# Performance work log

Hardware: AMD Instinct MI355X
Metric: run time of the kernel (lower is better)

Reference implementation:

```python
import jax, jax.numpy as jnp
import numpy as np
from jax import lax

B, M, L, D, V, H, DEC_HID = 1024, 4, 100, 512, 50000, 512, 128


def setup_inputs() -> dict:
    key = jax.random.key(0)
    ks = jax.random.split(key, 16)
    inputs = jax.random.randint(ks[0], (B, M, L), 0, V)
    masks = (jax.random.uniform(ks[1], (B, M)) > 0.3).astype(jnp.float32)
    embed_table = jax.random.normal(ks[2], (V, D), dtype=jnp.float32) * 0.02
    s_d = 1.0 / np.sqrt(D)
    s_h = 1.0 / np.sqrt(H)
    # torch nn.RNN params: h_t = relu(x W_ih^T + b_ih + h_{t-1} W_hh^T + b_hh)
    w_ih0 = jax.random.uniform(ks[3], (H, D), minval=-s_d, maxval=s_d)
    w_hh0 = jax.random.uniform(ks[4], (H, H), minval=-s_h, maxval=s_h)
    b_ih0 = jax.random.uniform(ks[5], (H,), minval=-s_h, maxval=s_h)
    b_hh0 = jax.random.uniform(ks[6], (H,), minval=-s_h, maxval=s_h)
    w_ih1 = jax.random.uniform(ks[7], (H, H), minval=-s_h, maxval=s_h)
    w_hh1 = jax.random.uniform(ks[8], (H, H), minval=-s_h, maxval=s_h)
    b_ih1 = jax.random.uniform(ks[9], (H,), minval=-s_h, maxval=s_h)
    b_hh1 = jax.random.uniform(ks[10], (H,), minval=-s_h, maxval=s_h)
    s_dec = 1.0 / np.sqrt(H)
    w_d1 = jax.random.uniform(ks[11], (DEC_HID, H), minval=-s_dec, maxval=s_dec)
    b_d1 = jax.random.uniform(ks[12], (DEC_HID,), minval=-s_dec, maxval=s_dec)
    s2 = 1.0 / np.sqrt(DEC_HID)
    w_d2 = jax.random.uniform(ks[13], (D, DEC_HID), minval=-s2, maxval=s2)
    b_d2 = jax.random.uniform(ks[14], (D,), minval=-s2, maxval=s2)
    return {"inputs": inputs, "masks": masks, "embed_table": embed_table,
            "w_ih0": w_ih0, "w_hh0": w_hh0, "b_ih0": b_ih0, "b_hh0": b_hh0,
            "w_ih1": w_ih1, "w_hh1": w_hh1, "b_ih1": b_ih1, "b_hh1": b_hh1,
            "w_d1": w_d1, "b_d1": b_d1, "w_d2": w_d2, "b_d2": b_d2}


def _masked_avg_pool(tok, emb, pad_token=0):
    # tok: (..., L) int; emb: (..., L, D)
    m = (tok != pad_token).astype(emb.dtype)
    pooled = (emb * m[..., None]).sum(axis=-2)
    denom = jnp.clip(m.sum(axis=-1, keepdims=True), 1.0, None)
    return pooled / denom


def reference(inputs, masks, embed_table,
              w_ih0, w_hh0, b_ih0, b_hh0,
              w_ih1, w_hh1, b_ih1, b_hh1,
              w_d1, b_d1, w_d2, b_d2):
    emb = embed_table[inputs]                       # (B, 4, L, D)
    past = jnp.array([3, 2, 0])
    x_past = _masked_avg_pool(inputs[:, past], emb[:, past])   # (B, 3, D)
    masks_past = masks[:, past]                                # (B, 3)
    x_future = _masked_avg_pool(inputs[:, 1], emb[:, 1])        # (B, D)

    b = inputs.shape[0]
    h_init = jnp.zeros((2, b, w_hh0.shape[0]), dtype=x_past.dtype)

    def step(h, xm):
        x_t, m_t = xm                               # (B, D), (B,)
        x_t = x_t * m_t[:, None]
        h0 = jax.nn.relu(x_t @ w_ih0.T + b_ih0 + h[0] @ w_hh0.T + b_hh0)
        h1 = jax.nn.relu(h0 @ w_ih1.T + b_ih1 + h[1] @ w_hh1.T + b_hh1)
        return jnp.stack([h0, h1]), None

    xs = (jnp.swapaxes(x_past, 0, 1), masks_past.T)  # scan over seq_len=3
    h_final, _ = lax.scan(step, h_init, xs)
    last_h = h_final[-1]                             # (B, H)

    x_future_hat = jax.nn.relu(last_h @ w_d1.T + b_d1) @ w_d2.T + b_d2
    return (x_future_hat, x_future, last_h)
```

## Files before the change

kernel.cpp:

```cpp
#include <hip/hip_runtime.h>
#include <hip/hip_bf16.h>

constexpr int NB   = 1024;
constexpr int NSEG = 4;
constexpr int LSEQ = 100;
constexpr int ND   = 512;
constexpr int NH   = 512;
constexpr int NDEC = 128;
constexpr size_t TBL_ELEMS = (size_t)50000 * ND;

typedef __attribute__((ext_vector_type(8))) short bf16x8;
typedef __attribute__((ext_vector_type(4))) float f32x4;
typedef __attribute__((ext_vector_type(2))) float f32x2;
typedef __attribute__((ext_vector_type(8))) unsigned short u16x8;

__device__ __forceinline__ ushort f2bf(float f) {
    union { float f; unsigned u; } v; v.f = f;
    unsigned r = (v.u + 0x7fffu + ((v.u >> 16) & 1u)) >> 16;
    return (ushort)r;
}
__device__ __forceinline__ float bf2f(ushort u) {
    return __uint_as_float((unsigned)u << 16);
}

#define GLOAD_LDS16(gp, lp)                                                     \
    __builtin_amdgcn_global_load_lds(                                           \
        (const __attribute__((address_space(1))) unsigned int*)(gp),            \
        (__attribute__((address_space(3))) unsigned int*)(lp), 16, 0, 0)

#define VMW(N) asm volatile("s_waitcnt vmcnt(" #N ")" ::: "memory")
#define RBAR() do { __builtin_amdgcn_s_barrier();                               \
                    __builtin_amdgcn_sched_barrier(0); } while (0)

__global__ __launch_bounds__(256)
void convert_all(const float* __restrict__ table,
                 const float* __restrict__ w_ih0, const float* __restrict__ w_hh0,
                 const float* __restrict__ w_ih1, const float* __restrict__ w_hh1,
                 const float* __restrict__ w_d1,  const float* __restrict__ w_d2,
                 const float* __restrict__ b_ih0, const float* __restrict__ b_hh0,
                 const float* __restrict__ b_ih1, const float* __restrict__ b_hh1,
                 unsigned* __restrict__ tb8, ushort* __restrict__ wbf,
                 float* __restrict__ bsum0, float* __restrict__ bsum1,
                 int doTable)
{
    const size_t stride = (size_t)gridDim.x * blockDim.x;
    const size_t gid    = (size_t)blockIdx.x * blockDim.x + threadIdx.x;

    if (doTable) {
        const size_t nvec = TBL_ELEMS / 8;
        for (size_t i = gid; i < nvec; i += stride) {
            const float4 a = ((const float4*)table)[2 * i];
            const float4 b = ((const float4*)table)[2 * i + 1];
            unsigned w0 = __builtin_amdgcn_cvt_pk_fp8_f32(a.x, a.y, 0, false);
            w0          = __builtin_amdgcn_cvt_pk_fp8_f32(a.z, a.w, w0, true);
            unsigned w1 = __builtin_amdgcn_cvt_pk_fp8_f32(b.x, b.y, 0, false);
            w1          = __builtin_amdgcn_cvt_pk_fp8_f32(b.z, b.w, w1, true);
            uint2 o; o.x = w0; o.y = w1;
            ((uint2*)tb8)[i] = o;
        }
    }
    constexpr int N0 = 512 * 512, ND2 = 128 * 512;
    constexpr int TOT = 4 * N0 + 2 * ND2 + 1024;
    for (size_t i = gid; i < TOT; i += stride) {
        if (i < 4 * (size_t)N0) {
            const float* src = (i < N0) ? w_ih0 : (i < 2*(size_t)N0) ? w_hh0
                             : (i < 3*(size_t)N0) ? w_ih1 : w_hh1;
            wbf[i] = f2bf(src[i & (N0 - 1)]);
        } else if (i < 4 * (size_t)N0 + ND2) {
            wbf[i] = f2bf(w_d1[i - 4 * (size_t)N0]);
        } else if (i < 4 * (size_t)N0 + 2 * ND2) {
            wbf[i] = f2bf(w_d2[i - 4 * (size_t)N0 - ND2]);
        } else {
            const int j = (int)(i - (4 * (size_t)N0 + 2 * ND2));
            if (j < 512) bsum0[j] = b_ih0[j] + b_hh0[j];
            else         bsum1[j - 512] = b_ih1[j - 512] + b_hh1[j - 512];
        }
    }
}

template<bool FP8>
__global__ __launch_bounds__(64)
void pool_kernel(const int* __restrict__ toks, const void* __restrict__ tbl,
                 const float* __restrict__ masks,
                 ushort* __restrict__ xpool, float* __restrict__ xfut)
{
    const int bm = blockIdx.x, m = bm & 3, lane = threadIdx.x;
    __shared__ int sidx[LSEQ];
    int cnt = 0;
    {
        const int t0 = toks[(size_t)bm * LSEQ + lane];
        const unsigned long long m0 = __ballot(t0 != 0);
        const int p0 = __popcll(m0 & ((1ull << lane) - 1ull));
        if (t0 != 0) sidx[p0] = t0;
        cnt = __popcll(m0);
        const int t1 = (lane < LSEQ - 64) ? toks[(size_t)bm * LSEQ + 64 + lane] : 0;
        const unsigned long long m1 = __ballot(t1 != 0);
        const int p1 = __popcll(m1 & ((1ull << lane) - 1ull));
        if (t1 != 0) sidx[cnt + p1] = t1;
        cnt += __popcll(m1);
    }
    __syncthreads();

    float acc[8] = {};
    int j = 0;
    if constexpr (FP8) {
        const unsigned char* tb = (const unsigned char*)tbl;
        const size_t off = (size_t)lane * 8;
        for (; j + 8 <= cnt; j += 8) {
            uint2 v[8];
            #pragma unroll
            for (int u = 0; u < 8; ++u)
                v[u] = *(const uint2*)&tb[(size_t)sidx[j + u] * ND + off];
            #pragma unroll
            for (int u = 0; u < 8; ++u) {
                const f32x2 p0 = __builtin_amdgcn_cvt_pk_f32_fp8(v[u].x, false);
                const f32x2 p1 = __builtin_amdgcn_cvt_pk_f32_fp8(v[u].x, true);
                const f32x2 p2 = __builtin_amdgcn_cvt_pk_f32_fp8(v[u].y, false);
                const f32x2 p3 = __builtin_amdgcn_cvt_pk_f32_fp8(v[u].y, true);
                acc[0] += p0[0]; acc[1] += p0[1]; acc[2] += p1[0]; acc[3] += p1[1];
                acc[4] += p2[0]; acc[5] += p2[1]; acc[6] += p3[0]; acc[7] += p3[1];
            }
        }
        for (; j < cnt; ++j) {
            const uint2 v = *(const uint2*)&tb[(size_t)sidx[j] * ND + off];
            const f32x2 p0 = __builtin_amdgcn_cvt_pk_f32_fp8(v.x, false);
            const f32x2 p1 = __builtin_amdgcn_cvt_pk_f32_fp8(v.x, true);
            const f32x2 p2 = __builtin_amdgcn_cvt_pk_f32_fp8(v.y, false);
            const f32x2 p3 = __builtin_amdgcn_cvt_pk_f32_fp8(v.y, true);
            acc[0] += p0[0]; acc[1] += p0[1]; acc[2] += p1[0]; acc[3] += p1[1];
            acc[4] += p2[0]; acc[5] += p2[1]; acc[6] += p3[0]; acc[7] += p3[1];
        }
    } else {
        const float* tb = (const float*)tbl;
        const int d = lane * 8;
        for (; j + 4 <= cnt; j += 4) {
            float4 v[4][2];
            #pragma unroll
            for (int u = 0; u < 4; ++u) {
                v[u][0] = *(const float4*)&tb[(size_t)sidx[j + u] * ND + d];
                v[u][1] = *(const float4*)&tb[(size_t)sidx[j + u] * ND + d + 4];
            }
            #pragma unroll
            for (int u = 0; u < 4; ++u) {
                acc[0] += v[u][0].x; acc[1] += v[u][0].y;
                acc[2] += v[u][0].z; acc[3] += v[u][0].w;
                acc[4] += v[u][1].x; acc[5] += v[u][1].y;
                acc[6] += v[u][1].z; acc[7] += v[u][1].w;
            }
        }
        for (; j < cnt; ++j) {
            const float4 a = *(const float4*)&tb[(size_t)sidx[j] * ND + d];
            const float4 b = *(const float4*)&tb[(size_t)sidx[j] * ND + d + 4];
            acc[0] += a.x; acc[1] += a.y; acc[2] += a.z; acc[3] += a.w;
            acc[4] += b.x; acc[5] += b.y; acc[6] += b.z; acc[7] += b.w;
        }
    }

    const float inv = 1.0f / (float)(cnt > 0 ? cnt : 1);
    const int d = lane * 8;
    if (m == 1) {
        float* dst = &xfut[(size_t)(bm >> 2) * ND + d];
        float4 o0 = {acc[0]*inv, acc[1]*inv, acc[2]*inv, acc[3]*inv};
        float4 o1 = {acc[4]*inv, acc[5]*inv, acc[6]*inv, acc[7]*inv};
        *(float4*)dst = o0; *(float4*)(dst + 4) = o1;
    } else {
        const float sc = masks[bm] * inv;
        u16x8 o;
        #pragma unroll
        for (int e = 0; e < 8; ++e) o[e] = f2bf(acc[e] * sc);
        *(u16x8*)&xpool[(size_t)bm * ND + d] = o;
    }
}

template<bool RELU, bool WF32, bool WBF>
__global__ __launch_bounds__(256)
void mfma_gemm(const ushort* __restrict__ A0, int lda0,
               const ushort* __restrict__ A1, int lda1,
               const ushort* __restrict__ W0, int ldw0,
               const ushort* __restrict__ W1, int ldw1,
               const float* __restrict__ bias,
               float* __restrict__ Cf, ushort* __restrict__ Cb, int ldc,
               int K0, int K1, int gx)
{
    __shared__ ushort SB[4][8192];
    const int tid  = threadIdx.x;
    const int lane = tid & 63;
    const int wid  = tid >> 6;
    const int l15  = lane & 15;
    const int sl   = lane >> 4;
    const int wr   = wid >> 1;
    const int wc   = wid & 1;

    const int per  = gridDim.x >> 3;
    const int tile = (blockIdx.x & 7) * per + (blockIdx.x >> 3);
    const int row0 = (tile / gx) * 64;
    const int col0 = (tile % gx) * 64;
    const int nt   = (K0 + K1) >> 6;

    f32x4 acc[2][2] = {};

    auto STAGE = [&](int t) {
        if (t >= nt) return;
        const int kg   = t * 64;
        const int ph   = (kg >= K0);
        const int koff = ph ? kg - K0 : kg;
        const ushort* Ap = ph ? A1 : A0;
        const int     la = ph ? lda1 : lda0;
        const ushort* Wp = ph ? W1 : W0;
        const int     lw = ph ? ldw1 : ldw0;
        ushort* dst = &SB[t & 3][0];
        const ushort* ga = Ap + (size_t)(row0 + wid * 16 + l15) * la + koff + sl * 8;
        GLOAD_LDS16(ga,      dst + (wid * 2 + 0) * 512);
        GLOAD_LDS16(ga + 32, dst + (wid * 2 + 1) * 512);
        const ushort* gw = Wp + (size_t)(col0 + wid * 16 + l15) * lw + koff + sl * 8;
        GLOAD_LDS16(gw,      dst + 4096 + (wid * 2 + 0) * 512);
        GLOAD_LDS16(gw + 32, dst + 4096 + (wid * 2 + 1) * 512);
    };

    auto COMPUTE = [&](int t) {
        const ushort* base = &SB[t & 3][0];
        #pragma unroll
        for (int ks = 0; ks < 2; ++ks) {
            const bf16x8 a0 = *(const bf16x8*)&base[((wr*2 + 0)*2 + ks)*512 + lane*8];
            const bf16x8 a1 = *(const bf16x8*)&base[((wr*2 + 1)*2 + ks)*512 + lane*8];
            const bf16x8 b0 = *(const bf16x8*)&base[4096 + ((wc*2 + 0)*2 + ks)*512 + lane*8];
            const bf16x8 b1 = *(const bf16x8*)&base[4096 + ((wc*2 + 1)*2 + ks)*512 + lane*8];
            acc[0][0] = __builtin_amdgcn_mfma_f32_16x16x32_bf16(a0, b0, acc[0][0], 0, 0, 0);
            acc[0][1] = __builtin_amdgcn_mfma_f32_16x16x32_bf16(a0, b1, acc[0][1], 0, 0, 0);
            acc[1][0] = __builtin_amdgcn_mfma_f32_16x16x32_bf16(a1, b0, acc[1][0], 0, 0, 0);
            acc[1][1] = __builtin_amdgcn_mfma_f32_16x16x32_bf16(a1, b1, acc[1][1], 0, 0, 0);
        }
    };

    STAGE(0); STAGE(1); STAGE(2);
    int t = 0;
    for (; t < nt - 3; ++t) {
        STAGE(t + 3);
        VMW(12); RBAR();
        COMPUTE(t);
        RBAR();
    }
    if (nt >= 3) { VMW(8); RBAR(); COMPUTE(nt - 3); }
    if (nt >= 2) { VMW(4); RBAR(); COMPUTE(nt - 2); }
    VMW(0); RBAR(); COMPUTE(nt - 1);

    #pragma unroll
    for (int fi = 0; fi < 2; ++fi)
        #pragma unroll
        for (int fj = 0; fj < 2; ++fj) {
            const int r0 = row0 + wr * 32 + fi * 16 + sl * 4;
            const int c  = col0 + wc * 32 + fj * 16 + l15;
            const float bb = bias ? bias[c] : 0.0f;
            #pragma unroll
            for (int r = 0; r < 4; ++r) {
                float v = acc[fi][fj][r] + bb;
                if (RELU) v = fmaxf(v, 0.0f);
                if (WF32) Cf[(size_t)(r0 + r) * ldc + c] = v;
                if (WBF)  Cb[(size_t)(r0 + r) * ldc + c] = f2bf(v);
            }
        }
}

extern "C" void kernel_launch(void* const* d_in, const int* in_sizes, int n_in,
                              void* d_out, int out_size, void* d_ws, size_t ws_size,
                              hipStream_t stream)
{
    (void)in_sizes; (void)n_in; (void)out_size;
    const int*   inputs = (const int*)  d_in[0];
    const float* masks  = (const float*)d_in[1];
    const float* embed  = (const float*)d_in[2];
    const float* w_ih0  = (const float*)d_in[3];
    const float* w_hh0  = (const float*)d_in[4];
    const float* b_ih0  = (const float*)d_in[5];
    const float* b_hh0  = (const float*)d_in[6];
    const float* w_ih1  = (const float*)d_in[7];
    const float* w_hh1  = (const float*)d_in[8];
    const float* b_ih1  = (const float*)d_in[9];
    const float* b_hh1  = (const float*)d_in[10];
    const float* w_d1   = (const float*)d_in[11];
    const float* b_d1   = (const float*)d_in[12];
    const float* w_d2   = (const float*)d_in[13];
    const float* b_d2   = (const float*)d_in[14];

    float* out    = (float*)d_out;
    float* xf_hat = out;
    float* xf     = out + (size_t)NB * ND;
    float* lasth  = out + 2 * (size_t)NB * ND;

    const size_t tbl_bytes  = TBL_ELEMS;
    const size_t rest_bytes = (size_t)1179648 * 2 + 4096
                            + (size_t)NB * NSEG * ND * 2
                            + 4 * (size_t)NB * NH * 2
                            + (size_t)NB * NDEC * 2;
    const bool bigws = ws_size >= tbl_bytes + rest_bytes + 1024;

    char* ws = (char*)d_ws;
    unsigned* tb8 = nullptr;
    if (bigws) { tb8 = (unsigned*)ws; ws += tbl_bytes; }
    ushort* wbf   = (ushort*)ws;  ws += (size_t)1179648 * 2;
    float*  bsum0 = (float*)ws;   ws += 2048;
    float*  bsum1 = (float*)ws;   ws += 2048;
    ushort* xpool = (ushort*)ws;  ws += (size_t)NB * NSEG * ND * 2;
    ushort* h0a   = (ushort*)ws;  ws += (size_t)NB * NH * 2;
    ushort* h0b   = (ushort*)ws;  ws += (size_t)NB * NH * 2;
    ushort* h1a   = (ushort*)ws;  ws += (size_t)NB * NH * 2;
    ushort* h1b   = (ushort*)ws;  ws += (size_t)NB * NH * 2;
    ushort* dec1b = (ushort*)ws;  ws += (size_t)NB * NDEC * 2;

    const ushort* wih0 = wbf;
    const ushort* whh0 = wbf + 262144;
    const ushort* wih1 = wbf + 524288;
    const ushort* whh1 = wbf + 786432;
    const ushort* wd1  = wbf + 1048576;
    const ushort* wd2  = wbf + 1114112;

    convert_all<<<2048, 256, 0, stream>>>(embed, w_ih0, w_hh0, w_ih1, w_hh1,
                                          w_d1, w_d2, b_ih0, b_hh0, b_ih1, b_hh1,
                                          tb8, wbf, bsum0, bsum1, bigws ? 1 : 0);
    if (bigws)
        pool_kernel<true ><<<NB * NSEG, 64, 0, stream>>>(inputs, tb8,   masks, xpool, xf);
    else
        pool_kernel<false><<<NB * NSEG, 64, 0, stream>>>(inputs, embed, masks, xpool, xf);

    const dim3 blk(256);
    const int nH  = (NH / 64)   * (NB / 64);
    const int nD1 = (NDEC / 64) * (NB / 64);
    const int nD2 = (ND / 64)   * (NB / 64);

    mfma_gemm<true,false,true><<<nH, blk, 0, stream>>>(
        xpool + 3 * ND, NSEG * ND, nullptr, 0, wih0, ND, nullptr, 0,
        bsum0, nullptr, h0a, NH, ND, 0, 8);
    mfma_gemm<true,false,true><<<nH, blk, 0, stream>>>(
        h0a, NH, nullptr, 0, wih1, NH, nullptr, 0,
        bsum1, nullptr, h1a, NH, NH, 0, 8);
    mfma_gemm<true,false,true><<<nH, blk, 0, stream>>>(
        xpool + 2 * ND, NSEG * ND, h0a, NH, wih0, ND, whh0, NH,
        bsum0, nullptr, h0b, NH, ND, NH, 8);
    mfma_gemm<true,false,true><<<nH, blk, 0, stream>>>(
        h0b, NH, h1a, NH, wih1, NH, whh1, NH,
        bsum1, nullptr, h1b, NH, NH, NH, 8);
    mfma_gemm<true,false,true><<<nH, blk, 0, stream>>>(
        xpool + 0 * ND, NSEG * ND, h0b, NH, wih0, ND, whh0, NH,
        bsum0, nullptr, h0a, NH, ND, NH, 8);
    mfma_gemm<true,true,true><<<nH, blk, 0, stream>>>(
        h0a, NH, h1b, NH, wih1, NH, whh1, NH,
        bsum1, lasth, h1a, NH, NH, NH, 8);

    mfma_gemm<true,false,true><<<nD1, blk, 0, stream>>>(
        h1a, NH, nullptr, 0, wd1, NH, nullptr, 0,
        b_d1, nullptr, dec1b, NDEC, NH, 0, 2);
    mfma_gemm<false,true,false><<<nD2, blk, 0, stream>>>(
        dec1b, NDEC, nullptr, 0, wd2, NDEC, nullptr, 0,
        b_d2, xf_hat, nullptr, ND, NDEC, 0, 8);
}
```

Before: 116.2 us.

## Split embedding pooling into vocab slices mapped to XCDs, then reduce partials

```diff
diff --git a/kernel.cpp b/kernel.cpp
--- a/kernel.cpp
+++ b/kernel.cpp
@@ -7,7 +7,10 @@
 constexpr int ND   = 512;
 constexpr int NH   = 512;
 constexpr int NDEC = 128;
-constexpr size_t TBL_ELEMS = (size_t)50000 * ND;
+constexpr int NV   = 50000;
+constexpr int NSLICE = 8;
+constexpr int SLICE_ROWS = NV / NSLICE;
+constexpr size_t TBL_ELEMS = (size_t)NV * ND;
 
 typedef __attribute__((ext_vector_type(8))) short bf16x8;
 typedef __attribute__((ext_vector_type(4))) float f32x4;
@@ -78,11 +81,122 @@
     }
 }
 
-template<bool FP8>
+__global__ __launch_bounds__(256)
+void poolA(const int* __restrict__ toks, const unsigned char* __restrict__ tb8,
+           const float* __restrict__ masks,
+           ushort* __restrict__ partial, unsigned* __restrict__ cnts)
+{
+    const int gid   = blockIdx.x;
+    const int slice = gid & 7;
+    const int wv    = threadIdx.x >> 6;
+    const int lane  = threadIdx.x & 63;
+    const int bm    = (gid >> 3) * 4 + wv;
+    const int m     = bm & 3;
+
+    __shared__ int sidx[4][112];
+    int* sw = sidx[wv];
+
+    if (m != 1 && masks[bm] == 0.0f) return;
+
+    const int lo = slice * SLICE_ROWS, hi = lo + SLICE_ROWS;
+    const unsigned long long lmlt = (1ull << lane) - 1ull;
+    int cnt;
+    {
+        const int t0 = __builtin_nontemporal_load(&toks[(size_t)bm * LSEQ + lane]);
+        const bool v0 = (t0 != 0) & (t0 >= lo) & (t0 < hi);
+        const unsigned long long b0 = __ballot(v0);
+        if (v0) sw[__popcll(b0 & lmlt)] = t0;
+        cnt = __popcll(b0);
+        int t1 = 0;
+        if (lane < LSEQ - 64)
+            t1 = __builtin_nontemporal_load(&toks[(size_t)bm * LSEQ + 64 + lane]);
+        const bool v1 = (t1 != 0) & (t1 >= lo) & (t1 < hi);
+        const unsigned long long b1 = __ballot(v1);
+        if (v1) sw[cnt + __popcll(b1 & lmlt)] = t1;
+        cnt += __popcll(b1);
+    }
+    asm volatile("s_waitcnt lgkmcnt(0)" ::: "memory");
+    __builtin_amdgcn_sched_barrier(0);
+
+    float acc[8] = {};
+    const size_t off = (size_t)lane * 8;
+    int j = 0;
+    for (; j + 4 <= cnt; j += 4) {
+        uint2 v[4];
+        #pragma unroll
+        for (int u = 0; u < 4; ++u)
+            v[u] = *(const uint2*)&tb8[(size_t)sw[j + u] * ND + off];
+        #pragma unroll
+        for (int u = 0; u < 4; ++u) {
+            const f32x2 p0 = __builtin_amdgcn_cvt_pk_f32_fp8(v[u].x, false);
+            const f32x2 p1 = __builtin_amdgcn_cvt_pk_f32_fp8(v[u].x, true);
+            const f32x2 p2 = __builtin_amdgcn_cvt_pk_f32_fp8(v[u].y, false);
+            const f32x2 p3 = __builtin_amdgcn_cvt_pk_f32_fp8(v[u].y, true);
+            acc[0] += p0[0]; acc[1] += p0[1]; acc[2] += p1[0]; acc[3] += p1[1];
+            acc[4] += p2[0]; acc[5] += p2[1]; acc[6] += p3[0]; acc[7] += p3[1];
+        }
+    }
+    for (; j < cnt; ++j) {
+        const uint2 v = *(const uint2*)&tb8[(size_t)sw[j] * ND + off];
+        const f32x2 p0 = __builtin_amdgcn_cvt_pk_f32_fp8(v.x, false);
+        const f32x2 p1 = __builtin_amdgcn_cvt_pk_f32_fp8(v.x, true);
+        const f32x2 p2 = __builtin_amdgcn_cvt_pk_f32_fp8(v.y, false);
+        const f32x2 p3 = __builtin_amdgcn_cvt_pk_f32_fp8(v.y, true);
+        acc[0] += p0[0]; acc[1] += p0[1]; acc[2] += p1[0]; acc[3] += p1[1];
+        acc[4] += p2[0]; acc[5] += p2[1]; acc[6] += p3[0]; acc[7] += p3[1];
+    }
+
+    u16x8 o;
+    #pragma unroll
+    for (int e = 0; e < 8; ++e) o[e] = f2bf(acc[e]);
+    __builtin_nontemporal_store(o,
+        (u16x8*)&partial[((size_t)bm * NSLICE + slice) * ND + lane * 8]);
+    if (lane == 0) cnts[bm * NSLICE + slice] = (unsigned)cnt;
+}
+
+__global__ __launch_bounds__(256)
+void poolB(const ushort* __restrict__ partial, const unsigned* __restrict__ cnts,
+           const float* __restrict__ masks,
+           ushort* __restrict__ xpool, float* __restrict__ xfut)
+{
+    const int bm   = blockIdx.x * 4 + (threadIdx.x >> 6);
+    const int lane = threadIdx.x & 63;
+    const int m    = bm & 3;
+    const int d    = lane * 8;
+
+    if (m != 1 && masks[bm] == 0.0f) {
+        u16x8 z = {};
+        *(u16x8*)&xpool[(size_t)bm * ND + d] = z;
+        return;
+    }
+    float acc[8] = {};
+    unsigned cnt = 0;
+    #pragma unroll
+    for (int jj = 0; jj < NSLICE; ++jj) {
+        const u16x8 p = __builtin_nontemporal_load(
+            (const u16x8*)&partial[((size_t)bm * NSLICE + jj) * ND + d]);
+        #pragma unroll
+        for (int e = 0; e < 8; ++e) acc[e] += bf2f(p[e]);
+        cnt += cnts[bm * NSLICE + jj];
+    }
+    const float inv = 1.0f / (float)(cnt > 0 ? cnt : 1);
+    if (m == 1) {
+        float* dst = &xfut[(size_t)(bm >> 2) * ND + d];
+        float4 o0 = {acc[0]*inv, acc[1]*inv, acc[2]*inv, acc[3]*inv};
+        float4 o1 = {acc[4]*inv, acc[5]*inv, acc[6]*inv, acc[7]*inv};
+        *(float4*)dst = o0; *(float4*)(dst + 4) = o1;
+    } else {
+        u16x8 o;
+        #pragma unroll
+        for (int e = 0; e < 8; ++e) o[e] = f2bf(acc[e] * inv);
+        *(u16x8*)&xpool[(size_t)bm * ND + d] = o;
+    }
+}
+
 __global__ __launch_bounds__(64)
-void pool_kernel(const int* __restrict__ toks, const void* __restrict__ tbl,
-                 const float* __restrict__ masks,
-                 ushort* __restrict__ xpool, float* __restrict__ xfut)
+void pool_fallback(const int* __restrict__ toks, const float* __restrict__ tb,
+                   const float* __restrict__ masks,
+                   ushort* __restrict__ xpool, float* __restrict__ xfut)
 {
     const int bm = blockIdx.x, m = bm & 3, lane = threadIdx.x;
     __shared__ int sidx[LSEQ];
@@ -100,64 +214,15 @@
         cnt += __popcll(m1);
     }
     __syncthreads();
-
+    const int d = lane * 8;
     float acc[8] = {};
-    int j = 0;
-    if constexpr (FP8) {
-        const unsigned char* tb = (const unsigned char*)tbl;
-        const size_t off = (size_t)lane * 8;
-        for (; j + 8 <= cnt; j += 8) {
-            uint2 v[8];
-            #pragma unroll
-            for (int u = 0; u < 8; ++u)
-                v[u] = *(const uint2*)&tb[(size_t)sidx[j + u] * ND + off];
-            #pragma unroll
-            for (int u = 0; u < 8; ++u) {
-                const f32x2 p0 = __builtin_amdgcn_cvt_pk_f32_fp8(v[u].x, false);
-                const f32x2 p1 = __builtin_amdgcn_cvt_pk_f32_fp8(v[u].x, true);
-                const f32x2 p2 = __builtin_amdgcn_cvt_pk_f32_fp8(v[u].y, false);
-                const f32x2 p3 = __builtin_amdgcn_cvt_pk_f32_fp8(v[u].y, true);
-                acc[0] += p0[0]; acc[1] += p0[1]; acc[2] += p1[0]; acc[3] += p1[1];
-                acc[4] += p2[0]; acc[5] += p2[1]; acc[6] += p3[0]; acc[7] += p3[1];
-            }
-        }
-        for (; j < cnt; ++j) {
-            const uint2 v = *(const uint2*)&tb[(size_t)sidx[j] * ND + off];
-            const f32x2 p0 = __builtin_amdgcn_cvt_pk_f32_fp8(v.x, false);
-            const f32x2 p1 = __builtin_amdgcn_cvt_pk_f32_fp8(v.x, true);
-            const f32x2 p2 = __builtin_amdgcn_cvt_pk_f32_fp8(v.y, false);
-            const f32x2 p3 = __builtin_amdgcn_cvt_pk_f32_fp8(v.y, true);
-            acc[0] += p0[0]; acc[1] += p0[1]; acc[2] += p1[0]; acc[3] += p1[1];
-            acc[4] += p2[0]; acc[5] += p2[1]; acc[6] += p3[0]; acc[7] += p3[1];
-        }
-    } else {
-        const float* tb = (const float*)tbl;
-        const int d = lane * 8;
-        for (; j + 4 <= cnt; j += 4) {
-            float4 v[4][2];
-            #pragma unroll
-            for (int u = 0; u < 4; ++u) {
-                v[u][0] = *(const float4*)&tb[(size_t)sidx[j + u] * ND + d];
-                v[u][1] = *(const float4*)&tb[(size_t)sidx[j + u] * ND + d + 4];
-            }
-            #pragma unroll
-            for (int u = 0; u < 4; ++u) {
-                acc[0] += v[u][0].x; acc[1] += v[u][0].y;
-                acc[2] += v[u][0].z; acc[3] += v[u][0].w;
-                acc[4] += v[u][1].x; acc[5] += v[u][1].y;
-                acc[6] += v[u][1].z; acc[7] += v[u][1].w;
-            }
-        }
-        for (; j < cnt; ++j) {
-            const float4 a = *(const float4*)&tb[(size_t)sidx[j] * ND + d];
-            const float4 b = *(const float4*)&tb[(size_t)sidx[j] * ND + d + 4];
-            acc[0] += a.x; acc[1] += a.y; acc[2] += a.z; acc[3] += a.w;
-            acc[4] += b.x; acc[5] += b.y; acc[6] += b.z; acc[7] += b.w;
-        }
-    }
-
+    for (int j = 0; j < cnt; ++j) {
+        const float4 a = *(const float4*)&tb[(size_t)sidx[j] * ND + d];
+        const float4 b = *(const float4*)&tb[(size_t)sidx[j] * ND + d + 4];
+        acc[0] += a.x; acc[1] += a.y; acc[2] += a.z; acc[3] += a.w;
+        acc[4] += b.x; acc[5] += b.y; acc[6] += b.z; acc[7] += b.w;
+    }
     const float inv = 1.0f / (float)(cnt > 0 ? cnt : 1);
-    const int d = lane * 8;
     if (m == 1) {
         float* dst = &xfut[(size_t)(bm >> 2) * ND + d];
         float4 o0 = {acc[0]*inv, acc[1]*inv, acc[2]*inv, acc[3]*inv};
@@ -288,15 +353,22 @@
     float* lasth  = out + 2 * (size_t)NB * ND;
 
     const size_t tbl_bytes  = TBL_ELEMS;
+    const size_t part_bytes = (size_t)NB * NSEG * NSLICE * ND * 2;
+    const size_t cnt_bytes  = (size_t)NB * NSEG * NSLICE * 4;
     const size_t rest_bytes = (size_t)1179648 * 2 + 4096
                             + (size_t)NB * NSEG * ND * 2
                             + 4 * (size_t)NB * NH * 2
                             + (size_t)NB * NDEC * 2;
-    const bool bigws = ws_size >= tbl_bytes + rest_bytes + 1024;
+    const bool bigws = ws_size >= tbl_bytes + part_bytes + cnt_bytes
+                                + rest_bytes + 1024;
 
     char* ws = (char*)d_ws;
-    unsigned* tb8 = nullptr;
-    if (bigws) { tb8 = (unsigned*)ws; ws += tbl_bytes; }
+    unsigned* tb8 = nullptr; ushort* partial = nullptr; unsigned* cnts = nullptr;
+    if (bigws) {
+        tb8     = (unsigned*)ws; ws += tbl_bytes;
+        partial = (ushort*)ws;   ws += part_bytes;
+        cnts    = (unsigned*)ws; ws += cnt_bytes;
+    }
     ushort* wbf   = (ushort*)ws;  ws += (size_t)1179648 * 2;
     float*  bsum0 = (float*)ws;   ws += 2048;
     float*  bsum1 = (float*)ws;   ws += 2048;
@@ -317,10 +389,13 @@
     convert_all<<<2048, 256, 0, stream>>>(embed, w_ih0, w_hh0, w_ih1, w_hh1,
                                           w_d1, w_d2, b_ih0, b_hh0, b_ih1, b_hh1,
                                           tb8, wbf, bsum0, bsum1, bigws ? 1 : 0);
-    if (bigws)
-        pool_kernel<true ><<<NB * NSEG, 64, 0, stream>>>(inputs, tb8,   masks, xpool, xf);
-    else
-        pool_kernel<false><<<NB * NSEG, 64, 0, stream>>>(inputs, embed, masks, xpool, xf);
+    if (bigws) {
+        poolA<<<(NB * NSEG / 4) * NSLICE, 256, 0, stream>>>(
+            inputs, (const unsigned char*)tb8, masks, partial, cnts);
+        poolB<<<NB * NSEG / 4, 256, 0, stream>>>(partial, cnts, masks, xpool, xf);
+    } else {
+        pool_fallback<<<NB * NSEG, 64, 0, stream>>>(inputs, embed, masks, xpool, xf);
+    }
 
     const dim3 blk(256);
     const int nH  = (NH / 64)   * (NB / 64);
```

Result: slower. 122.0 us (+5.0%).

## Batch independent RNN GEMMs into shared launches and skip pooling for masked segments

Applied to the files above, without the earlier changes.

```diff
diff --git a/kernel.cpp b/kernel.cpp
--- a/kernel.cpp
+++ b/kernel.cpp
@@ -7,7 +7,8 @@
 constexpr int ND   = 512;
 constexpr int NH   = 512;
 constexpr int NDEC = 128;
-constexpr size_t TBL_ELEMS = (size_t)50000 * ND;
+constexpr int NV   = 50000;
+constexpr size_t TBL_ELEMS = (size_t)NV * ND;
 
 typedef __attribute__((ext_vector_type(8))) short bf16x8;
 typedef __attribute__((ext_vector_type(4))) float f32x4;
@@ -78,14 +79,93 @@
     }
 }
 
-template<bool FP8>
 __global__ __launch_bounds__(64)
-void pool_kernel(const int* __restrict__ toks, const void* __restrict__ tbl,
-                 const float* __restrict__ masks,
-                 ushort* __restrict__ xpool, float* __restrict__ xfut)
+void pool_fp8(const int* __restrict__ toks, const unsigned char* __restrict__ tb8,
+              const float* __restrict__ masks,
+              ushort* __restrict__ xpool, float* __restrict__ xfut)
 {
     const int bm = blockIdx.x, m = bm & 3, lane = threadIdx.x;
-    __shared__ int sidx[LSEQ];
+    const int d  = lane * 8;
+
+    if (m != 1 && masks[bm] == 0.0f) {
+        u16x8 z = {};
+        *(u16x8*)&xpool[(size_t)bm * ND + d] = z;
+        return;
+    }
+
+    __shared__ int sidx[112];
+    int cnt = 0;
+    {
+        const int t0 = __builtin_nontemporal_load(&toks[(size_t)bm * LSEQ + lane]);
+        const unsigned long long m0 = __ballot(t0 != 0);
+        const int p0 = __popcll(m0 & ((1ull << lane) - 1ull));
+        if (t0 != 0) sidx[p0] = t0;
+        cnt = __popcll(m0);
+        int t1 = 0;
+        if (lane < LSEQ - 64)
+            t1 = __builtin_nontemporal_load(&toks[(size_t)bm * LSEQ + 64 + lane]);
+        const unsigned long long m1 = __ballot(t1 != 0);
+        const int p1 = __popcll(m1 & ((1ull << lane) - 1ull));
+        if (t1 != 0) sidx[cnt + p1] = t1;
+        cnt += __popcll(m1);
+    }
+    __syncthreads();
+
+    float acc[8] = {};
+    const size_t off = (size_t)lane * 8;
+    int j = 0;
+    for (; j + 8 <= cnt; j += 8) {
+        uint2 v[8];
+        #pragma unroll
+        for (int u = 0; u < 8; ++u)
+            v[u] = *(const uint2*)&tb8[(size_t)sidx[j + u] * ND + off];
+        #pragma unroll
+        for (int u = 0; u < 8; ++u) {
+            const f32x2 p0 = __builtin_amdgcn_cvt_pk_f32_fp8(v[u].x, false);
+            const f32x2 p1 = __builtin_amdgcn_cvt_pk_f32_fp8(v[u].x, true);
+            const f32x2 p2 = __builtin_amdgcn_cvt_pk_f32_fp8(v[u].y, false);
+            const f32x2 p3 = __builtin_amdgcn_cvt_pk_f32_fp8(v[u].y, true);
+            acc[0] += p0[0]; acc[1] += p0[1]; acc[2] += p1[0]; acc[3] += p1[1];
+            acc[4] += p2[0]; acc[5] += p2[1]; acc[6] += p3[0]; acc[7] += p3[1];
+        }
+    }
+    for (; j < cnt; ++j) {
+        const uint2 v = *(const uint2*)&tb8[(size_t)sidx[j] * ND + off];
+        const f32x2 p0 = __builtin_amdgcn_cvt_pk_f32_fp8(v.x, false);
+        const f32x2 p1 = __builtin_amdgcn_cvt_pk_f32_fp8(v.x, true);
+        const f32x2 p2 = __builtin_amdgcn_cvt_pk_f32_fp8(v.y, false);
+        const f32x2 p3 = __builtin_amdgcn_cvt_pk_f32_fp8(v.y, true);
+        acc[0] += p0[0]; acc[1] += p0[1]; acc[2] += p1[0]; acc[3] += p1[1];
+        acc[4] += p2[0]; acc[5] += p2[1]; acc[6] += p3[0]; acc[7] += p3[1];
+    }
+
+    const float inv = 1.0f / (float)(cnt > 0 ? cnt : 1);
+    if (m == 1) {
+        float* dst = &xfut[(size_t)(bm >> 2) * ND + d];
+        float4 o0 = {acc[0]*inv, acc[1]*inv, acc[2]*inv, acc[3]*inv};
+        float4 o1 = {acc[4]*inv, acc[5]*inv, acc[6]*inv, acc[7]*inv};
+        *(float4*)dst = o0; *(float4*)(dst + 4) = o1;
+    } else {
+        u16x8 o;
+        #pragma unroll
+        for (int e = 0; e < 8; ++e) o[e] = f2bf(acc[e] * inv);
+        *(u16x8*)&xpool[(size_t)bm * ND + d] = o;
+    }
+}
+
+__global__ __launch_bounds__(64)
+void pool_fallback(const int* __restrict__ toks, const float* __restrict__ tb,
+                   const float* __restrict__ masks,
+                   ushort* __restrict__ xpool, float* __restrict__ xfut)
+{
+    const int bm = blockIdx.x, m = bm & 3, lane = threadIdx.x;
+    const int d  = lane * 8;
+    if (m != 1 && masks[bm] == 0.0f) {
+        u16x8 z = {};
+        *(u16x8*)&xpool[(size_t)bm * ND + d] = z;
+        return;
+    }
+    __shared__ int sidx[112];
     int cnt = 0;
     {
         const int t0 = toks[(size_t)bm * LSEQ + lane];
@@ -100,89 +180,45 @@
         cnt += __popcll(m1);
     }
     __syncthreads();
-
     float acc[8] = {};
-    int j = 0;
-    if constexpr (FP8) {
-        const unsigned char* tb = (const unsigned char*)tbl;
-        const size_t off = (size_t)lane * 8;
-        for (; j + 8 <= cnt; j += 8) {
-            uint2 v[8];
-            #pragma unroll
-            for (int u = 0; u < 8; ++u)
-                v[u] = *(const uint2*)&tb[(size_t)sidx[j + u] * ND + off];
-            #pragma unroll
-            for (int u = 0; u < 8; ++u) {
-                const f32x2 p0 = __builtin_amdgcn_cvt_pk_f32_fp8(v[u].x, false);
-                const f32x2 p1 = __builtin_amdgcn_cvt_pk_f32_fp8(v[u].x, true);
-                const f32x2 p2 = __builtin_amdgcn_cvt_pk_f32_fp8(v[u].y, false);
-                const f32x2 p3 = __builtin_amdgcn_cvt_pk_f32_fp8(v[u].y, true);
-                acc[0] += p0[0]; acc[1] += p0[1]; acc[2] += p1[0]; acc[3] += p1[1];
-                acc[4] += p2[0]; acc[5] += p2[1]; acc[6] += p3[0]; acc[7] += p3[1];
-            }
-        }
-        for (; j < cnt; ++j) {
-            const uint2 v = *(const uint2*)&tb[(size_t)sidx[j] * ND + off];
-            const f32x2 p0 = __builtin_amdgcn_cvt_pk_f32_fp8(v.x, false);
-            const f32x2 p1 = __builtin_amdgcn_cvt_pk_f32_fp8(v.x, true);
-            const f32x2 p2 = __builtin_amdgcn_cvt_pk_f32_fp8(v.y, false);
-            const f32x2 p3 = __builtin_amdgcn_cvt_pk_f32_fp8(v.y, true);
-            acc[0] += p0[0]; acc[1] += p0[1]; acc[2] += p1[0]; acc[3] += p1[1];
-            acc[4] += p2[0]; acc[5] += p2[1]; acc[6] += p3[0]; acc[7] += p3[1];
-        }
-    } else {
-        const float* tb = (const float*)tbl;
-        const int d = lane * 8;
-        for (; j + 4 <= cnt; j += 4) {
-            float4 v[4][2];
-            #pragma unroll
-            for (int u = 0; u < 4; ++u) {
-                v[u][0] = *(const float4*)&tb[(size_t)sidx[j + u] * ND + d];
-                v[u][1] = *(const float4*)&tb[(size_t)sidx[j + u] * ND + d + 4];
-            }
-            #pragma unroll
-            for (int u = 0; u < 4; ++u) {
-                acc[0] += v[u][0].x; acc[1] += v[u][0].y;
-                acc[2] += v[u][0].z; acc[3] += v[u][0].w;
-                acc[4] += v[u][1].x; acc[5] += v[u][1].y;
-                acc[6] += v[u][1].z; acc[7] += v[u][1].w;
-            }
-        }
-        for (; j < cnt; ++j) {
-            const float4 a = *(const float4*)&tb[(size_t)sidx[j] * ND + d];
-            const float4 b = *(const float4*)&tb[(size_t)sidx[j] * ND + d + 4];
-            acc[0] += a.x; acc[1] += a.y; acc[2] += a.z; acc[3] += a.w;
-            acc[4] += b.x; acc[5] += b.y; acc[6] += b.z; acc[7] += b.w;
-        }
-    }
-
+    for (int j = 0; j < cnt; ++j) {
+        const float4 a = *(const float4*)&tb[(size_t)sidx[j] * ND + d];
+        const float4 b = *(const float4*)&tb[(size_t)sidx[j] * ND + d + 4];
+        acc[0] += a.x; acc[1] += a.y; acc[2] += a.z; acc[3] += a.w;
+        acc[4] += b.x; acc[5] += b.y; acc[6] += b.z; acc[7] += b.w;
+    }
     const float inv = 1.0f / (float)(cnt > 0 ? cnt : 1);
-    const int d = lane * 8;
     if (m == 1) {
         float* dst = &xfut[(size_t)(bm >> 2) * ND + d];
         float4 o0 = {acc[0]*inv, acc[1]*inv, acc[2]*inv, acc[3]*inv};
         float4 o1 = {acc[4]*inv, acc[5]*inv, acc[6]*inv, acc[7]*inv};
         *(float4*)dst = o0; *(float4*)(dst + 4) = o1;
     } else {
-        const float sc = masks[bm] * inv;
         u16x8 o;
         #pragma unroll
-        for (int e = 0; e < 8; ++e) o[e] = f2bf(acc[e] * sc);
+        for (int e = 0; e < 8; ++e) o[e] = f2bf(acc[e] * inv);
         *(u16x8*)&xpool[(size_t)bm * ND + d] = o;
     }
 }
+
+struct GDesc {
+    const ushort *A0, *A1, *W0, *W1;
+    const float  *bias;
+    float        *Cf;
+    ushort       *Cb;
+    int lda0, lda1, ldw0, ldw1, ldc, K0, K1, gx;
+};
 
 template<bool RELU, bool WF32, bool WBF>
 __global__ __launch_bounds__(256)
-void mfma_gemm(const ushort* __restrict__ A0, int lda0,
-               const ushort* __restrict__ A1, int lda1,
-               const ushort* __restrict__ W0, int ldw0,
-               const ushort* __restrict__ W1, int ldw1,
-               const float* __restrict__ bias,
-               float* __restrict__ Cf, ushort* __restrict__ Cb, int ldc,
-               int K0, int K1, int gx)
+void mfma_gemm2(GDesc da, GDesc db, int n0)
 {
     __shared__ ushort SB[4][8192];
+    const bool second = ((int)blockIdx.x >= n0);
+    const GDesc d   = second ? db : da;
+    const int   lb  = second ? (int)blockIdx.x - n0 : (int)blockIdx.x;
+    const int  nloc = second ? (int)gridDim.x - n0 : n0;
+
     const int tid  = threadIdx.x;
     const int lane = tid & 63;
     const int wid  = tid >> 6;
@@ -191,23 +227,23 @@
     const int wr   = wid >> 1;
     const int wc   = wid & 1;
 
-    const int per  = gridDim.x >> 3;
-    const int tile = (blockIdx.x & 7) * per + (blockIdx.x >> 3);
-    const int row0 = (tile / gx) * 64;
-    const int col0 = (tile % gx) * 64;
-    const int nt   = (K0 + K1) >> 6;
+    const int per  = nloc >> 3;
+    const int tile = (lb & 7) * per + (lb >> 3);
+    const int row0 = (tile / d.gx) * 64;
+    const int col0 = (tile % d.gx) * 64;
+    const int nt   = (d.K0 + d.K1) >> 6;
 
     f32x4 acc[2][2] = {};
 
     auto STAGE = [&](int t) {
         if (t >= nt) return;
         const int kg   = t * 64;
-        const int ph   = (kg >= K0);
-        const int koff = ph ? kg - K0 : kg;
-        const ushort* Ap = ph ? A1 : A0;
-        const int     la = ph ? lda1 : lda0;
-        const ushort* Wp = ph ? W1 : W0;
-        const int     lw = ph ? ldw1 : ldw0;
+        const int ph   = (kg >= d.K0);
+        const int koff = ph ? kg - d.K0 : kg;
+        const ushort* Ap = ph ? d.A1 : d.A0;
+        const int     la = ph ? d.lda1 : d.lda0;
+        const ushort* Wp = ph ? d.W1 : d.W0;
+        const int     lw = ph ? d.ldw1 : d.ldw0;
         ushort* dst = &SB[t & 3][0];
         const ushort* ga = Ap + (size_t)(row0 + wid * 16 + l15) * la + koff + sl * 8;
         GLOAD_LDS16(ga,      dst + (wid * 2 + 0) * 512);
@@ -250,13 +286,13 @@
         for (int fj = 0; fj < 2; ++fj) {
             const int r0 = row0 + wr * 32 + fi * 16 + sl * 4;
             const int c  = col0 + wc * 32 + fj * 16 + l15;
-            const float bb = bias ? bias[c] : 0.0f;
+            const float bb = d.bias ? d.bias[c] : 0.0f;
             #pragma unroll
             for (int r = 0; r < 4; ++r) {
                 float v = acc[fi][fj][r] + bb;
                 if (RELU) v = fmaxf(v, 0.0f);
-                if (WF32) Cf[(size_t)(r0 + r) * ldc + c] = v;
-                if (WBF)  Cb[(size_t)(r0 + r) * ldc + c] = f2bf(v);
+                if (WF32) d.Cf[(size_t)(r0 + r) * d.ldc + c] = v;
+                if (WBF)  d.Cb[(size_t)(r0 + r) * d.ldc + c] = f2bf(v);
             }
         }
 }
@@ -318,38 +354,47 @@
                                           w_d1, w_d2, b_ih0, b_hh0, b_ih1, b_hh1,
                                           tb8, wbf, bsum0, bsum1, bigws ? 1 : 0);
     if (bigws)
-        pool_kernel<true ><<<NB * NSEG, 64, 0, stream>>>(inputs, tb8,   masks, xpool, xf);
+        pool_fp8<<<NB * NSEG, 64, 0, stream>>>(inputs, (const unsigned char*)tb8,
+                                               masks, xpool, xf);
     else
-        pool_kernel<false><<<NB * NSEG, 64, 0, stream>>>(inputs, embed, masks, xpool, xf);
+        pool_fallback<<<NB * NSEG, 64, 0, stream>>>(inputs, embed, masks, xpool, xf);
 
     const dim3 blk(256);
     const int nH  = (NH / 64)   * (NB / 64);
     const int nD1 = (NDEC / 64) * (NB / 64);
     const int nD2 = (ND / 64)   * (NB / 64);
 
-    mfma_gemm<true,false,true><<<nH, blk, 0, stream>>>(
-        xpool + 3 * ND, NSEG * ND, nullptr, 0, wih0, ND, nullptr, 0,
-        bsum0, nullptr, h0a, NH, ND, 0, 8);
-    mfma_gemm<true,false,true><<<nH, blk, 0, stream>>>(
-        h0a, NH, nullptr, 0, wih1, NH, nullptr, 0,
-        bsum1, nullptr, h1a, NH, NH, 0, 8);
-    mfma_gemm<true,false,true><<<nH, blk, 0, stream>>>(
-        xpool + 2 * ND, NSEG * ND, h0a, NH, wih0, ND, whh0, NH,
-        bsum0, nullptr, h0b, NH, ND, NH, 8);
-    mfma_gemm<true,false,true><<<nH, blk, 0, stream>>>(
-        h0b, NH, h1a, NH, wih1, NH, whh1, NH,
-        bsum1, nullptr, h1b, NH, NH, NH, 8);
-    mfma_gemm<true,false,true><<<nH, blk, 0, stream>>>(
-        xpool + 0 * ND, NSEG * ND, h0b, NH, wih0, ND, whh0, NH,
-        bsum0, nullptr, h0a, NH, ND, NH, 8);
-    mfma_gemm<true,true,true><<<nH, blk, 0, stream>>>(
-        h0a, NH, h1b, NH, wih1, NH, whh1, NH,
-        bsum1, lasth, h1a, NH, NH, NH, 8);
-
-    mfma_gemm<true,false,true><<<nD1, blk, 0, stream>>>(
-        h1a, NH, nullptr, 0, wd1, NH, nullptr, 0,
-        b_d1, nullptr, dec1b, NDEC, NH, 0, 2);
-    mfma_gemm<false,true,false><<<nD2, blk, 0, stream>>>(
-        dec1b, NDEC, nullptr, 0, wd2, NDEC, nullptr, 0,
-        b_d2, xf_hat, nullptr, ND, NDEC, 0, 8);
-}
+    auto mk = [](const ushort* A0, int lda0, const ushort* A1, int lda1,
+                 const ushort* W0, int ldw0, const ushort* W1, int ldw1,
+                 const float* bias, float* Cf, ushort* Cb, int ldc,
+                 int K0, int K1, int gx) {
+        GDesc g; g.A0 = A0; g.A1 = A1; g.W0 = W0; g.W1 = W1; g.bias = bias;
+        g.Cf = Cf; g.Cb = Cb; g.lda0 = lda0; g.lda1 = lda1; g.ldw0 = ldw0;
+        g.ldw1 = ldw1; g.ldc = ldc; g.K0 = K0; g.K1 = K1; g.gx = gx;
+        return g;
+    };
+
+    const GDesc G1 = mk(xpool + 3 * ND, NSEG * ND, nullptr, 0,
+                        wih0, ND, nullptr, 0, bsum0, nullptr, h0a, NH, ND, 0, 8);
+    const GDesc G2 = mk(h0a, NH, nullptr, 0,
+                        wih1, NH, nullptr, 0, bsum1, nullptr, h1a, NH, NH, 0, 8);
+    const GDesc G3 = mk(xpool + 2 * ND, NSEG * ND, h0a, NH,
+                        wih0, ND, whh0, NH, bsum0, nullptr, h0b, NH, ND, NH, 8);
+    const GDesc G4 = mk(h0b, NH, h1a, NH,
+                        wih1, NH, whh1, NH, bsum1, nullptr, h1b, NH, NH, NH, 8);
+    const GDesc G5 = mk(xpool + 0 * ND, NSEG * ND, h0b, NH,
+                        wih0, ND, whh0, NH, bsum0, nullptr, h0a, NH, ND, NH, 8);
+    const GDesc G6 = mk(h0a, NH, h1b, NH,
+                        wih1, NH, whh1, NH, bsum1, lasth, h1a, NH, NH, NH, 8);
+    const GDesc D1 = mk(h1a, NH, nullptr, 0,
+                        wd1, NH, nullptr, 0, b_d1, nullptr, dec1b, NDEC, NH, 0, 2);
+    const GDesc D2 = mk(dec1b, NDEC, nullptr, 0,
+                        wd2, NDEC, nullptr, 0, b_d2, xf_hat, nullptr, ND, NDEC, 0, 8);
+
+    mfma_gemm2<true,false,true><<<nH,      blk, 0, stream>>>(G1, G1, nH);
+    mfma_gemm2<true,false,true><<<2 * nH,  blk, 0, stream>>>(G2, G3, nH);
+    mfma_gemm2<true,false,true><<<2 * nH,  blk, 0, stream>>>(G4, G5, nH);
+    mfma_gemm2<true,true, true><<<nH,      blk, 0, stream>>>(G6, G6, nH);
+    mfma_gemm2<true,false,true><<<nD1,     blk, 0, stream>>>(D1, D1, nD1);
+    mfma_gemm2<false,true,false><<<nD2,    blk, 0, stream>>>(D2, D2, nD2);
+}
```

Result: faster. 100.5 us (-13.5%).
